# Performance work log

Measured on AMD Instinct MI355X. Metric: run time of the kernel, lower is better.

## Reference

```python
import jax, jax.numpy as jnp
import numpy as np

N = 100000   # nodes
E = 3200000  # edges
C = 256      # in_channels
H = 64       # hidden_channels
G = 512      # graphs in batch
FC = [128, 64, 32, 16]
OUT = 2
EPS = 1e-5


def _linear(key, fan_in, fan_out):
    k1, k2 = jax.random.split(key)
    s = 1.0 / np.sqrt(fan_in)
    W = jax.random.uniform(k1, (fan_in, fan_out), jnp.float32, -s, s)
    b = jax.random.uniform(k2, (fan_out,), jnp.float32, -s, s)
    return W, b


def setup_inputs() -> dict:
    key = jax.random.key(0)
    ks = jax.random.split(key, 12)
    x = jax.random.normal(ks[0], (N, C), jnp.float32)
    edge_index = jax.random.randint(ks[1], (2, E), 0, N, dtype=jnp.int64)
    batch = jnp.sort(jax.random.randint(ks[2], (N,), 0, G, dtype=jnp.int64))
    w1, b1 = _linear(ks[3], C, H)
    w2, b2 = _linear(ks[4], H, H)
    g1 = jnp.ones((H,), jnp.float32); be1 = jnp.zeros((H,), jnp.float32)
    g2 = jnp.ones((H,), jnp.float32); be2 = jnp.zeros((H,), jnp.float32)
    fw1, fb1 = _linear(ks[5], H, FC[0])
    fw2, fb2 = _linear(ks[6], FC[0], FC[1])
    fw3, fb3 = _linear(ks[7], FC[1], FC[2])
    fw4, fb4 = _linear(ks[8], FC[2], FC[3])
    ow, ob = _linear(ks[9], FC[3], OUT)
    return dict(x=x, edge_index=edge_index, batch=batch,
                w1=w1, b1=b1, w2=w2, b2=b2,
                g1=g1, be1=be1, g2=g2, be2=be2,
                fw1=fw1, fb1=fb1, fw2=fw2, fb2=fb2,
                fw3=fw3, fb3=fb3, fw4=fw4, fb4=fb4,
                ow=ow, ob=ob)


def _gcn_layers(x, edge_index, w1, b1, w2, b2, g1, be1, g2, be2):
    # PyG GCNConv: add self loops, symmetric deg^-1/2 normalization, scatter-add at dst
    loops = jnp.arange(N, dtype=edge_index.dtype)
    src = jnp.concatenate([edge_index[0], loops])
    dst = jnp.concatenate([edge_index[1], loops])
    deg = jax.ops.segment_sum(jnp.ones((E + N,), jnp.float32), dst, num_segments=N)
    dis = jnp.where(deg > 0, jax.lax.rsqrt(jnp.maximum(deg, 1.0)), 0.0)
    norm = (dis[src] * dis[dst])[:, None]  # [E+N, 1]

    def conv(h, W, b):
        h = h @ W
        return jax.ops.segment_sum(h[src] * norm, dst, num_segments=N) + b

    def bn(h, g, be):  # BatchNorm1d over node dim (training-mode batch stats)
        m = jnp.mean(h, axis=0)
        v = jnp.var(h, axis=0)
        return (h - m) * jax.lax.rsqrt(v + EPS) * g + be

    h = bn(jax.nn.relu(conv(x, w1, b1)), g1, be1)   # dropout = identity (eval)
    h = bn(jax.nn.relu(conv(h, w2, b2)), g2, be2)
    return h


def reference(x, edge_index, batch, w1, b1, w2, b2, g1, be1, g2, be2,
              fw1, fb1, fw2, fb2, fw3, fb3, fw4, fb4, ow, ob):
    h = _gcn_layers(x, edge_index, w1, b1, w2, b2, g1, be1, g2, be2)
    # global_mean_pool over batch vector
    s = jax.ops.segment_sum(h, batch, num_segments=G)
    cnt = jax.ops.segment_sum(jnp.ones((N,), jnp.float32), batch, num_segments=G)
    p = s / jnp.maximum(cnt, 1.0)[:, None]  # [G, H]
    h = jax.nn.relu(p @ fw1 + fb1)
    h = jax.nn.relu(h @ fw2 + fb2)
    h = jax.nn.relu(h @ fw3 + fb3)
    h = jax.nn.relu(h @ fw4 + fb4)
    return h @ ow + ob  # [G, OUT]
```

## Files before the change

### kernel.cpp

```cpp
#include <hip/hip_runtime.h>
#include <hip/hip_fp16.h>

#define N_NODES 100000
#define E_EDGES 3200000
#define NG      512
#define BN_EPS  1e-5f

#define BSH     7
#define BNODES  128
#define NBUCK   782
#define NCHUNK  1024
#define CHUNK   3125

__global__ __launch_bounds__(256) void k_zero(float* __restrict__ stats1,
                                              float* __restrict__ stats2,
                                              float* __restrict__ sums,
                                              float* __restrict__ cnt) {
  int i = blockIdx.x * 256 + threadIdx.x;
  if (i < 128) { stats1[i] = 0.f; stats2[i] = 0.f; }
  if (i < NG * 64) sums[i] = 0.f;
  if (i < NG) cnt[i] = 0.f;
}

__global__ __launch_bounds__(256) void kb_hist(const int* __restrict__ ei,
                                               int* __restrict__ counts) {
  __shared__ int h[NBUCK];
  const int c = blockIdx.x, tid = threadIdx.x;
  for (int b = tid; b < NBUCK; b += 256) h[b] = 0;
  __syncthreads();
  const int* dst = ei + E_EDGES + c * CHUNK;
  for (int i = tid; i < CHUNK; i += 256) atomicAdd(&h[dst[i] >> BSH], 1);
  __syncthreads();
  for (int b = tid; b < NBUCK; b += 256) counts[b * NCHUNK + c] = h[b];
}

__global__ __launch_bounds__(1024) void kb_scan1(int* __restrict__ counts,
                                                 int* __restrict__ btot) {
  __shared__ int sm[NCHUNK];
  const int b = blockIdx.x, tid = threadIdx.x;
  const int cval = counts[b * NCHUNK + tid];
  int val = cval;
  sm[tid] = val;
  __syncthreads();
  for (int off = 1; off < NCHUNK; off <<= 1) {
    int t = (tid >= off) ? sm[tid - off] : 0;
    __syncthreads();
    val += t;
    sm[tid] = val;
    __syncthreads();
  }
  counts[b * NCHUNK + tid] = val - cval;
  if (tid == NCHUNK - 1) btot[b] = val;
}

__global__ __launch_bounds__(1024) void kb_scan2(const int* __restrict__ btot,
                                                 int* __restrict__ bbase) {
  __shared__ int sm[1024];
  const int tid = threadIdx.x;
  const int cval = (tid < NBUCK) ? btot[tid] : 0;
  int val = cval;
  sm[tid] = val;
  __syncthreads();
  for (int off = 1; off < 1024; off <<= 1) {
    int t = (tid >= off) ? sm[tid - off] : 0;
    __syncthreads();
    val += t;
    sm[tid] = val;
    __syncthreads();
  }
  if (tid < NBUCK) bbase[tid] = val - cval;
  if (tid == NBUCK - 1) bbase[NBUCK] = val;
}

__global__ __launch_bounds__(256) void kb_scatter(const int* __restrict__ ei,
                                                  const int* __restrict__ counts,
                                                  const int* __restrict__ bbase,
                                                  int* __restrict__ binned) {
  __shared__ int cur[NBUCK];
  const int c = blockIdx.x, tid = threadIdx.x;
  for (int b = tid; b < NBUCK; b += 256) cur[b] = bbase[b] + counts[b * NCHUNK + c];
  __syncthreads();
  const int* srcp = ei + c * CHUNK;
  const int* dstp = ei + E_EDGES + c * CHUNK;
  for (int i = tid; i < CHUNK; i += 256) {
    const int s = srcp[i], d = dstp[i];
    const int pos = atomicAdd(&cur[d >> BSH], 1);
    binned[pos] = ((d & (BNODES - 1)) << 17) | s;
  }
}

__global__ __launch_bounds__(256) void kb_degsort(const int* __restrict__ binned,
                                                  const int* __restrict__ bbase,
                                                  int* __restrict__ csr,
                                                  int* __restrict__ row_start,
                                                  float* __restrict__ dis) {
  __shared__ int h[BNODES];
  __shared__ int pre[BNODES];
  const int b = blockIdx.x, tid = threadIdx.x;
  if (tid < BNODES) h[tid] = 0;
  __syncthreads();
  const int e0 = bbase[b], e1 = bbase[b + 1];
  for (int i = e0 + tid; i < e1; i += 256) atomicAdd(&h[binned[i] >> 17], 1);
  __syncthreads();
  if (tid < BNODES) pre[tid] = h[tid];
  __syncthreads();
  for (int off = 1; off < BNODES; off <<= 1) {
    int t = (tid >= off && tid < BNODES) ? pre[tid - off] : 0;
    __syncthreads();
    if (tid < BNODES) pre[tid] += t;
    __syncthreads();
  }
  if (tid < BNODES) {
    const int n = b * BNODES + tid;
    const int ex = e0 + pre[tid] - h[tid];
    if (n < N_NODES) {
      row_start[n] = ex;
      dis[n] = rsqrtf((float)(h[tid] + 1));
    }
    h[tid] = ex;
  }
  if (b == NBUCK - 1 && tid == 0) row_start[N_NODES] = E_EDGES;
  __syncthreads();
  for (int i = e0 + tid; i < e1; i += 256) {
    const int v = binned[i];
    const int pos = atomicAdd(&h[v >> 17], 1);
    csr[pos] = v & 0x1FFFF;
  }
}

template <int K, bool BN>
__global__ __launch_bounds__(256) void k_gemm(const float* __restrict__ in,
                                              const float* __restrict__ W,
                                              const float* __restrict__ dis,
                                              const float* __restrict__ stats,
                                              const float* __restrict__ gam,
                                              const float* __restrict__ bet,
                                              __half* __restrict__ y) {
  __shared__ float xs[64 * 68];
  __shared__ float wsm[64 * 64];
  __shared__ float scv[64], shv[64];
  const int tid = threadIdx.x;
  const int n0 = blockIdx.x * 64;
  const int lane = tid & 63, wv = tid >> 6;
  const int nq = lane & 15;
  const int chb = wv * 16 + (lane >> 4) * 4;
  if (BN) {
    if (tid < 64) {
      const float m = stats[tid] * (1.0f / N_NODES);
      const float v = stats[64 + tid] * (1.0f / N_NODES) - m * m;
      const float sc = rsqrtf(v + BN_EPS) * gam[tid];
      scv[tid] = sc;
      shv[tid] = bet[tid] - m * sc;
    }
  }
  float a[4][4] = {{0,0,0,0},{0,0,0,0},{0,0,0,0},{0,0,0,0}};
  for (int c0 = 0; c0 < K; c0 += 64) {
    __syncthreads();
#pragma unroll
    for (int i = 0; i < 4; ++i) {
      const int idx = tid + i * 256;
      const int n = idx >> 4, c4 = (idx & 15) * 4;
      const int nn = min(n0 + n, N_NODES - 1);
      float4 v = *(const float4*)&in[(size_t)nn * K + c0 + c4];
      if (BN) {
        v.x = v.x * scv[c4] + shv[c4];
        v.y = v.y * scv[c4 + 1] + shv[c4 + 1];
        v.z = v.z * scv[c4 + 2] + shv[c4 + 2];
        v.w = v.w * scv[c4 + 3] + shv[c4 + 3];
      }
      *(float4*)&xs[n * 68 + c4] = v;
    }
#pragma unroll
    for (int i = 0; i < 4; ++i) {
      const int idx = tid + i * 256;
      const int c = idx >> 4, ch4 = (idx & 15) * 4;
      *(float4*)&wsm[c * 64 + ch4] = *(const float4*)&W[(size_t)(c0 + c) * 64 + ch4];
    }
    __syncthreads();
    for (int c = 0; c < 64; c += 4) {
      float wq[4][4];
#pragma unroll
      for (int cc = 0; cc < 4; ++cc) {
        const float4 w4 = *(const float4*)&wsm[(c + cc) * 64 + chb];
        wq[cc][0] = w4.x; wq[cc][1] = w4.y; wq[cc][2] = w4.z; wq[cc][3] = w4.w;
      }
#pragma unroll
      for (int i = 0; i < 4; ++i) {
        const float4 xv = *(const float4*)&xs[(nq + 16 * i) * 68 + c];
#pragma unroll
        for (int j = 0; j < 4; ++j) {
          a[i][j] = fmaf(xv.x, wq[0][j],
                    fmaf(xv.y, wq[1][j],
                    fmaf(xv.z, wq[2][j],
                    fmaf(xv.w, wq[3][j], a[i][j]))));
        }
      }
    }
  }
#pragma unroll
  for (int i = 0; i < 4; ++i) {
    const int n = n0 + nq + 16 * i;
    if (n < N_NODES) {
      const float d = dis[n];
      union { __half h[4]; float2 f; } u;
      u.h[0] = __float2half_rn(d * a[i][0]);
      u.h[1] = __float2half_rn(d * a[i][1]);
      u.h[2] = __float2half_rn(d * a[i][2]);
      u.h[3] = __float2half_rn(d * a[i][3]);
      *(float2*)&y[(size_t)n * 64 + chb] = u.f;
    }
  }
}

template <bool POOL>
__global__ __launch_bounds__(256) void k_gather(const int* __restrict__ csr,
                                                const int* __restrict__ rs,
                                                const __half* __restrict__ y,
                                                const float* __restrict__ dis,
                                                const float* __restrict__ bias,
                                                float* __restrict__ hout,
                                                float* __restrict__ stats,
                                                const int* __restrict__ batch,
                                                float* __restrict__ sums,
                                                float* __restrict__ cnt) {
  const int tid = threadIdx.x;
  const int lane = tid & 63;
  const int p = lane >> 5;
  const int c = lane & 31;
  const int wid = (blockIdx.x * 256 + tid) >> 6;
  const int nw = (gridDim.x * 256) >> 6;
  const int per = (N_NODES + nw - 1) / nw;
  const int n0 = wid * per;
  const int n1 = min(N_NODES, n0 + per);
  const float bx = bias[2 * c], by = bias[2 * c + 1];
  float s1x = 0.f, s1y = 0.f, s2x = 0.f, s2y = 0.f;
  int curg = -1, run = 0;
  float px = 0.f, py = 0.f;
  for (int n = n0; n < n1; ++n) {
    int e = rs[n];
    const int end = rs[n + 1];
    float ax = 0.f, ay = 0.f;
    if (p == 0) {
      const float2 f = __half22float2(*(const __half2*)&y[(size_t)n * 64 + 2 * c]);
      ax = f.x; ay = f.y;
    }
    for (; e + 8 <= end; e += 8) {
      const int i0 = csr[e + p];
      const int i1 = csr[e + 2 + p];
      const int i2 = csr[e + 4 + p];
      const int i3 = csr[e + 6 + p];
      const float2 f0 = __half22float2(*(const __half2*)&y[(size_t)i0 * 64 + 2 * c]);
      const float2 f1 = __half22float2(*(const __half2*)&y[(size_t)i1 * 64 + 2 * c]);
      const float2 f2 = __half22float2(*(const __half2*)&y[(size_t)i2 * 64 + 2 * c]);
      const float2 f3 = __half22float2(*(const __half2*)&y[(size_t)i3 * 64 + 2 * c]);
      ax += (f0.x + f1.x) + (f2.x + f3.x);
      ay += (f0.y + f1.y) + (f2.y + f3.y);
    }
    for (; e + 2 <= end; e += 2) {
      const int i0 = csr[e + p];
      const float2 f = __half22float2(*(const __half2*)&y[(size_t)i0 * 64 + 2 * c]);
      ax += f.x; ay += f.y;
    }
    if (e < end && p == 0) {
      const int i0 = csr[e];
      const float2 f = __half22float2(*(const __half2*)&y[(size_t)i0 * 64 + 2 * c]);
      ax += f.x; ay += f.y;
    }
    ax += __shfl_xor(ax, 32);
    ay += __shfl_xor(ay, 32);
    const float d = dis[n];
    const float vx = fmaxf(d * ax + bx, 0.f);
    const float vy = fmaxf(d * ay + by, 0.f);
    if (lane < 32) {
      if (!POOL) *(float2*)&hout[(size_t)n * 64 + 2 * c] = make_float2(vx, vy);
      s1x += vx; s1y += vy;
      s2x += vx * vx; s2y += vy * vy;
    }
    if (POOL) {
      const int g = batch[n];
      if (g != curg) {
        if (run) {
          if (lane < 32) {
            atomicAdd(&sums[curg * 64 + 2 * c], px);
            atomicAdd(&sums[curg * 64 + 2 * c + 1], py);
          }
          if (lane == 0) atomicAdd(&cnt[curg], (float)run);
        }
        curg = g; run = 0; px = 0.f; py = 0.f;
      }
      if (lane < 32) { px += vx; py += vy; }
      ++run;
    }
  }
  if (POOL && run) {
    if (lane < 32) {
      atomicAdd(&sums[curg * 64 + 2 * c], px);
      atomicAdd(&sums[curg * 64 + 2 * c + 1], py);
    }
    if (lane == 0) atomicAdd(&cnt[curg], (float)run);
  }
  __shared__ float r1[256], r2[256];
  const int wv = tid >> 6;
  if (lane < 32) {
    r1[wv * 64 + 2 * c] = s1x; r1[wv * 64 + 2 * c + 1] = s1y;
    r2[wv * 64 + 2 * c] = s2x; r2[wv * 64 + 2 * c + 1] = s2y;
  }
  __syncthreads();
  if (tid < 64) {
    atomicAdd(&stats[tid], r1[tid] + r1[tid + 64] + r1[tid + 128] + r1[tid + 192]);
  } else if (tid < 128) {
    const int h = tid - 64;
    atomicAdd(&stats[64 + h], r2[h] + r2[h + 64] + r2[h + 128] + r2[h + 192]);
  }
}

__global__ __launch_bounds__(128) void k_mlp(const float* __restrict__ sums,
                                             const float* __restrict__ cnt,
                                             const float* __restrict__ stats,
                                             const float* __restrict__ gam,
                                             const float* __restrict__ bet,
                                             const float* __restrict__ fw1, const float* __restrict__ fb1,
                                             const float* __restrict__ fw2, const float* __restrict__ fb2,
                                             const float* __restrict__ fw3, const float* __restrict__ fb3,
                                             const float* __restrict__ fw4, const float* __restrict__ fb4,
                                             const float* __restrict__ ow, const float* __restrict__ ob,
                                             float* __restrict__ out) {
  __shared__ float u0[128], u1[128];
  const int g = blockIdx.x, t = threadIdx.x;
  if (t < 64) {
    const float m = stats[t] * (1.0f / N_NODES);
    const float v = stats[64 + t] * (1.0f / N_NODES) - m * m;
    const float sc = rsqrtf(v + BN_EPS) * gam[t];
    const float sh = bet[t] - m * sc;
    u0[t] = (sums[g * 64 + t] / fmaxf(cnt[g], 1.0f)) * sc + sh;
  }
  __syncthreads();
  if (t < 128) {
    float a = fb1[t];
    for (int k = 0; k < 64; ++k) a = fmaf(u0[k], fw1[k * 128 + t], a);
    u1[t] = fmaxf(a, 0.f);
  }
  __syncthreads();
  if (t < 64) {
    float a = fb2[t];
    for (int k = 0; k < 128; ++k) a = fmaf(u1[k], fw2[k * 64 + t], a);
    u0[t] = fmaxf(a, 0.f);
  }
  __syncthreads();
  if (t < 32) {
    float a = fb3[t];
    for (int k = 0; k < 64; ++k) a = fmaf(u0[k], fw3[k * 32 + t], a);
    u1[t] = fmaxf(a, 0.f);
  }
  __syncthreads();
  if (t < 16) {
    float a = fb4[t];
    for (int k = 0; k < 32; ++k) a = fmaf(u1[k], fw4[k * 16 + t], a);
    u0[t] = fmaxf(a, 0.f);
  }
  __syncthreads();
  if (t < 2) {
    float a = ob[t];
    for (int k = 0; k < 16; ++k) a = fmaf(u0[k], ow[k * 2 + t], a);
    out[g * 2 + t] = a;
  }
}

extern "C" void kernel_launch(void* const* d_in, const int* in_sizes, int n_in,
                              void* d_out, int out_size, void* d_ws, size_t ws_size,
                              hipStream_t stream) {
  const float* x    = (const float*)d_in[0];
  const int*   ei   = (const int*)d_in[1];
  const int*   batch= (const int*)d_in[2];
  const float* w1   = (const float*)d_in[3];
  const float* b1   = (const float*)d_in[4];
  const float* w2   = (const float*)d_in[5];
  const float* b2   = (const float*)d_in[6];
  const float* g1   = (const float*)d_in[7];
  const float* be1  = (const float*)d_in[8];
  const float* g2   = (const float*)d_in[9];
  const float* be2  = (const float*)d_in[10];
  const float* fw1  = (const float*)d_in[11]; const float* fb1 = (const float*)d_in[12];
  const float* fw2  = (const float*)d_in[13]; const float* fb2 = (const float*)d_in[14];
  const float* fw3  = (const float*)d_in[15]; const float* fb3 = (const float*)d_in[16];
  const float* fw4  = (const float*)d_in[17]; const float* fb4 = (const float*)d_in[18];
  const float* ow   = (const float*)d_in[19]; const float* ob  = (const float*)d_in[20];
  float* out = (float*)d_out;

  char* ws = (char*)d_ws;
  auto alloc = [&](size_t bytes) {
    void* p = ws;
    ws += (bytes + 255) & ~(size_t)255;
    return p;
  };
  float*  dis      = (float*)alloc((size_t)N_NODES * 4);
  int*    counts   = (int*)  alloc((size_t)NBUCK * NCHUNK * 4);
  int*    btot     = (int*)  alloc((size_t)NBUCK * 4);
  int*    bbase    = (int*)  alloc((size_t)(NBUCK + 1) * 4);
  int*    binned   = (int*)  alloc((size_t)E_EDGES * 4);
  int*    csr      = (int*)  alloc((size_t)E_EDGES * 4);
  int*    row_start= (int*)  alloc((size_t)(N_NODES + 1) * 4);
  __half* yH       = (__half*)alloc((size_t)N_NODES * 64 * 2);
  float*  hB       = (float*)alloc((size_t)N_NODES * 64 * 4);
  float*  stats1   = (float*)alloc(512);
  float*  stats2   = (float*)alloc(512);
  float*  sums     = (float*)alloc((size_t)NG * 64 * 4);
  float*  cnt      = (float*)alloc((size_t)NG * 4);

  const int nblkG = (N_NODES + 63) / 64;

  k_zero    <<<128, 256, 0, stream>>>(stats1, stats2, sums, cnt);
  kb_hist   <<<NCHUNK, 256, 0, stream>>>(ei, counts);
  kb_scan1  <<<NBUCK, NCHUNK, 0, stream>>>(counts, btot);
  kb_scan2  <<<1, 1024, 0, stream>>>(btot, bbase);
  kb_scatter<<<NCHUNK, 256, 0, stream>>>(ei, counts, bbase, binned);
  kb_degsort<<<NBUCK, 256, 0, stream>>>(binned, bbase, csr, row_start, dis);

  k_gemm<256, false><<<nblkG, 256, 0, stream>>>(x, w1, dis, nullptr, nullptr, nullptr, yH);
  k_gather<false><<<2048, 256, 0, stream>>>(csr, row_start, yH, dis, b1, hB, stats1,
                                            nullptr, nullptr, nullptr);

  k_gemm<64, true><<<nblkG, 256, 0, stream>>>(hB, w2, dis, stats1, g1, be1, yH);
  k_gather<true><<<2048, 256, 0, stream>>>(csr, row_start, yH, dis, b2, nullptr, stats2,
                                           batch, sums, cnt);

  k_mlp<<<NG, 128, 0, stream>>>(sums, cnt, stats2, g2, be2,
                                fw1, fb1, fw2, fb2, fw3, fb3, fw4, fb4, ow, ob, out);
}
```

Measured before the change: 600.6 us.

## Gather fp16 rows with 16-byte loads over 8 edges per wave

Changes the per-node gather so each lane loads 8 half-precision channels with one 16-byte load, and a wave covers 8 edges in parallel instead of 2 with 4-byte loads. Partial sums across the 8 edge groups are combined with a three-step butterfly shuffle that ends with each lane owning one channel, so all 64 lanes write outputs and stats. This cuts the number of load instructions per gathered row and raises memory-level parallelism on the random neighbour reads. In exchange it adds shuffle and select work per node and wastes lanes on nodes with few neighbours.

```diff
diff --git a/kernel.cpp b/kernel.cpp
--- a/kernel.cpp
+++ b/kernel.cpp
@@ -225,86 +225,114 @@
                                                 float* __restrict__ cnt) {
   const int tid = threadIdx.x;
   const int lane = tid & 63;
-  const int p = lane >> 5;
-  const int c = lane & 31;
+  const int p = lane >> 3;
+  const int c8 = lane & 7;
+  const int ch = c8 * 8 + ((p & 1) << 2) + (p & 2) + ((p >> 2) & 1);
   const int wid = (blockIdx.x * 256 + tid) >> 6;
   const int nw = (gridDim.x * 256) >> 6;
   const int per = (N_NODES + nw - 1) / nw;
   const int n0 = wid * per;
   const int n1 = min(N_NODES, n0 + per);
-  const float bx = bias[2 * c], by = bias[2 * c + 1];
-  float s1x = 0.f, s1y = 0.f, s2x = 0.f, s2y = 0.f;
+  const float bch = bias[ch];
+  float s1 = 0.f, s2 = 0.f;
   int curg = -1, run = 0;
-  float px = 0.f, py = 0.f;
+  float px = 0.f;
+  union U8 { float4 f4; __half2 h2[4]; };
   for (int n = n0; n < n1; ++n) {
     int e = rs[n];
     const int end = rs[n + 1];
-    float ax = 0.f, ay = 0.f;
+    float acc[8] = {0.f, 0.f, 0.f, 0.f, 0.f, 0.f, 0.f, 0.f};
     if (p == 0) {
-      const float2 f = __half22float2(*(const __half2*)&y[(size_t)n * 64 + 2 * c]);
-      ax = f.x; ay = f.y;
+      U8 u;
+      u.f4 = *(const float4*)&y[(size_t)n * 64 + c8 * 8];
+#pragma unroll
+      for (int q = 0; q < 4; ++q) {
+        const float2 f = __half22float2(u.h2[q]);
+        acc[2 * q] += f.x;
+        acc[2 * q + 1] += f.y;
+      }
+    }
+    for (; e + 16 <= end; e += 16) {
+      const int ia = csr[e + p];
+      const int ib = csr[e + 8 + p];
+      U8 ua, ub;
+      ua.f4 = *(const float4*)&y[(size_t)ia * 64 + c8 * 8];
+      ub.f4 = *(const float4*)&y[(size_t)ib * 64 + c8 * 8];
+#pragma unroll
+      for (int q = 0; q < 4; ++q) {
+        const float2 fa = __half22float2(ua.h2[q]);
+        const float2 fb = __half22float2(ub.h2[q]);
+        acc[2 * q] += fa.x + fb.x;
+        acc[2 * q + 1] += fa.y + fb.y;
+      }
     }
     for (; e + 8 <= end; e += 8) {
-      const int i0 = csr[e + p];
-      const int i1 = csr[e + 2 + p];
-      const int i2 = csr[e + 4 + p];
-      const int i3 = csr[e + 6 + p];
-      const float2 f0 = __half22float2(*(const __half2*)&y[(size_t)i0 * 64 + 2 * c]);
-      const float2 f1 = __half22float2(*(const __half2*)&y[(size_t)i1 * 64 + 2 * c]);
-      const float2 f2 = __half22float2(*(const __half2*)&y[(size_t)i2 * 64 + 2 * c]);
-      const float2 f3 = __half22float2(*(const __half2*)&y[(size_t)i3 * 64 + 2 * c]);
-      ax += (f0.x + f1.x) + (f2.x + f3.x);
-      ay += (f0.y + f1.y) + (f2.y + f3.y);
-    }
-    for (; e + 2 <= end; e += 2) {
-      const int i0 = csr[e + p];
-      const float2 f = __half22float2(*(const __half2*)&y[(size_t)i0 * 64 + 2 * c]);
-      ax += f.x; ay += f.y;
-    }
-    if (e < end && p == 0) {
-      const int i0 = csr[e];
-      const float2 f = __half22float2(*(const __half2*)&y[(size_t)i0 * 64 + 2 * c]);
-      ax += f.x; ay += f.y;
-    }
-    ax += __shfl_xor(ax, 32);
-    ay += __shfl_xor(ay, 32);
-    const float d = dis[n];
-    const float vx = fmaxf(d * ax + bx, 0.f);
-    const float vy = fmaxf(d * ay + by, 0.f);
-    if (lane < 32) {
-      if (!POOL) *(float2*)&hout[(size_t)n * 64 + 2 * c] = make_float2(vx, vy);
-      s1x += vx; s1y += vy;
-      s2x += vx * vx; s2y += vy * vy;
-    }
+      const int ia = csr[e + p];
+      U8 ua;
+      ua.f4 = *(const float4*)&y[(size_t)ia * 64 + c8 * 8];
+#pragma unroll
+      for (int q = 0; q < 4; ++q) {
+        const float2 fa = __half22float2(ua.h2[q]);
+        acc[2 * q] += fa.x;
+        acc[2 * q + 1] += fa.y;
+      }
+    }
+    if (e < end) {
+      const int rem = end - e;
+      const int i0 = csr[(p < rem) ? e + p : e];
+      U8 u;
+      u.f4 = *(const float4*)&y[(size_t)i0 * 64 + c8 * 8];
+      if (p < rem) {
+#pragma unroll
+        for (int q = 0; q < 4; ++q) {
+          const float2 f = __half22float2(u.h2[q]);
+          acc[2 * q] += f.x;
+          acc[2 * q + 1] += f.y;
+        }
+      }
+    }
+    float t[4];
+#pragma unroll
+    for (int j = 0; j < 4; ++j) {
+      const float send = (p & 1) ? acc[j] : acc[4 + j];
+      const float keep = (p & 1) ? acc[4 + j] : acc[j];
+      t[j] = keep + __shfl_xor(send, 8);
+    }
+    float u2[2];
+#pragma unroll
+    for (int j = 0; j < 2; ++j) {
+      const float send = (p & 2) ? t[j] : t[2 + j];
+      const float keep = (p & 2) ? t[2 + j] : t[j];
+      u2[j] = keep + __shfl_xor(send, 16);
+    }
+    const float send3 = (p & 4) ? u2[0] : u2[1];
+    const float keep3 = (p & 4) ? u2[1] : u2[0];
+    const float s = keep3 + __shfl_xor(send3, 32);
+    const float v = fmaxf(dis[n] * s + bch, 0.f);
+    if (!POOL) hout[(size_t)n * 64 + ch] = v;
+    s1 += v;
+    s2 += v * v;
     if (POOL) {
       const int g = batch[n];
       if (g != curg) {
         if (run) {
-          if (lane < 32) {
-            atomicAdd(&sums[curg * 64 + 2 * c], px);
-            atomicAdd(&sums[curg * 64 + 2 * c + 1], py);
-          }
+          atomicAdd(&sums[curg * 64 + ch], px);
           if (lane == 0) atomicAdd(&cnt[curg], (float)run);
         }
-        curg = g; run = 0; px = 0.f; py = 0.f;
-      }
-      if (lane < 32) { px += vx; py += vy; }
+        curg = g; run = 0; px = 0.f;
+      }
+      px += v;
       ++run;
     }
   }
   if (POOL && run) {
-    if (lane < 32) {
-      atomicAdd(&sums[curg * 64 + 2 * c], px);
-      atomicAdd(&sums[curg * 64 + 2 * c + 1], py);
-    }
+    atomicAdd(&sums[curg * 64 + ch], px);
     if (lane == 0) atomicAdd(&cnt[curg], (float)run);
   }
   __shared__ float r1[256], r2[256];
   const int wv = tid >> 6;
-  if (lane < 32) {
-    r1[wv * 64 + 2 * c] = s1x; r1[wv * 64 + 2 * c + 1] = s1y;
-    r2[wv * 64 + 2 * c] = s2x; r2[wv * 64 + 2 * c + 1] = s2y;
-  }
+  r1[wv * 64 + ch] = s1;
+  r2[wv * 64 + ch] = s2;
   __syncthreads();
   if (tid < 64) {
     atomicAdd(&stats[tid], r1[tid] + r1[tid + 64] + r1[tid + 128] + r1[tid + 192]);
```

After: 568.8 us. -5.3%, faster.

## Split gather into channel slices with 16 edges per wave iteration

Applied to the files above, without the earlier changes.

Rewrites the neighbour-aggregation kernel so each block works on one of four 16-channel slices. Each lane loads 8 bytes (four halves) for one of 16 edges at a time, instead of two lanes per edge covering all 64 channels. The aim is to keep more independent neighbour loads in flight and shrink each block's per-row working set of the feature table. The cost is that CSR indices and the per-node loop run four times, once per slice. The block-to-slice and node-range mapping is hardcoded for a fixed grid size, so it depends on the launch matching it.

```diff
diff --git a/kernel.cpp b/kernel.cpp
--- a/kernel.cpp
+++ b/kernel.cpp
@@ -223,94 +223,124 @@
                                                 const int* __restrict__ batch,
                                                 float* __restrict__ sums,
                                                 float* __restrict__ cnt) {
-  const int tid = threadIdx.x;
+  const int tid  = threadIdx.x;
   const int lane = tid & 63;
-  const int p = lane >> 5;
-  const int c = lane & 31;
-  const int wid = (blockIdx.x * 256 + tid) >> 6;
-  const int nw = (gridDim.x * 256) >> 6;
-  const int per = (N_NODES + nw - 1) / nw;
-  const int n0 = wid * per;
-  const int n1 = min(N_NODES, n0 + per);
-  const float bx = bias[2 * c], by = bias[2 * c + 1];
-  float s1x = 0.f, s1y = 0.f, s2x = 0.f, s2y = 0.f;
+  const int slot = lane >> 2;
+  const int cq   = lane & 3;
+  const int slice = (blockIdx.x & 7) >> 1;
+  const int sbase = slice * 16;
+  const int chl  = cq * 4 + (slot & 3);
+  const int ch   = sbase + chl;
+  const int j    = ((blockIdx.x >> 3) << 1) | (blockIdx.x & 1);
+  const int wid  = j * 4 + (tid >> 6);
+  const int per  = (N_NODES + 2047) / 2048;
+  const int n0   = wid * per;
+  const int n1   = min(N_NODES, n0 + per);
+  const float bch = bias[ch];
+  const __half* yb = y + sbase + cq * 4;
+  float s1 = 0.f, s2 = 0.f;
   int curg = -1, run = 0;
-  float px = 0.f, py = 0.f;
+  float px = 0.f;
+  union U4 { float2 f2; __half2 h2[2]; };
   for (int n = n0; n < n1; ++n) {
     int e = rs[n];
     const int end = rs[n + 1];
-    float ax = 0.f, ay = 0.f;
-    if (p == 0) {
-      const float2 f = __half22float2(*(const __half2*)&y[(size_t)n * 64 + 2 * c]);
-      ax = f.x; ay = f.y;
-    }
-    for (; e + 8 <= end; e += 8) {
-      const int i0 = csr[e + p];
-      const int i1 = csr[e + 2 + p];
-      const int i2 = csr[e + 4 + p];
-      const int i3 = csr[e + 6 + p];
-      const float2 f0 = __half22float2(*(const __half2*)&y[(size_t)i0 * 64 + 2 * c]);
-      const float2 f1 = __half22float2(*(const __half2*)&y[(size_t)i1 * 64 + 2 * c]);
-      const float2 f2 = __half22float2(*(const __half2*)&y[(size_t)i2 * 64 + 2 * c]);
-      const float2 f3 = __half22float2(*(const __half2*)&y[(size_t)i3 * 64 + 2 * c]);
-      ax += (f0.x + f1.x) + (f2.x + f3.x);
-      ay += (f0.y + f1.y) + (f2.y + f3.y);
-    }
-    for (; e + 2 <= end; e += 2) {
-      const int i0 = csr[e + p];
-      const float2 f = __half22float2(*(const __half2*)&y[(size_t)i0 * 64 + 2 * c]);
-      ax += f.x; ay += f.y;
-    }
-    if (e < end && p == 0) {
-      const int i0 = csr[e];
-      const float2 f = __half22float2(*(const __half2*)&y[(size_t)i0 * 64 + 2 * c]);
-      ax += f.x; ay += f.y;
-    }
-    ax += __shfl_xor(ax, 32);
-    ay += __shfl_xor(ay, 32);
-    const float d = dis[n];
-    const float vx = fmaxf(d * ax + bx, 0.f);
-    const float vy = fmaxf(d * ay + by, 0.f);
-    if (lane < 32) {
-      if (!POOL) *(float2*)&hout[(size_t)n * 64 + 2 * c] = make_float2(vx, vy);
-      s1x += vx; s1y += vy;
-      s2x += vx * vx; s2y += vy * vy;
+    float a0 = 0.f, a1 = 0.f, a2 = 0.f, a3 = 0.f;
+    if (slot == 0) {
+      U4 u;
+      u.f2 = *(const float2*)&yb[(size_t)n * 64];
+      const float2 f0 = __half22float2(u.h2[0]);
+      const float2 f1 = __half22float2(u.h2[1]);
+      a0 += f0.x; a1 += f0.y; a2 += f1.x; a3 += f1.y;
+    }
+    for (; e + 32 <= end; e += 32) {
+      const int ia = __builtin_nontemporal_load(&csr[e + slot]);
+      const int ib = __builtin_nontemporal_load(&csr[e + 16 + slot]);
+      U4 ua, ub;
+      ua.f2 = *(const float2*)&yb[(size_t)ia * 64];
+      ub.f2 = *(const float2*)&yb[(size_t)ib * 64];
+      const float2 fa0 = __half22float2(ua.h2[0]);
+      const float2 fa1 = __half22float2(ua.h2[1]);
+      const float2 fb0 = __half22float2(ub.h2[0]);
+      const float2 fb1 = __half22float2(ub.h2[1]);
+      a0 += fa0.x + fb0.x; a1 += fa0.y + fb0.y;
+      a2 += fa1.x + fb1.x; a3 += fa1.y + fb1.y;
+    }
+    for (; e + 16 <= end; e += 16) {
+      const int ia = __builtin_nontemporal_load(&csr[e + slot]);
+      U4 ua;
+      ua.f2 = *(const float2*)&yb[(size_t)ia * 64];
+      const float2 fa0 = __half22float2(ua.h2[0]);
+      const float2 fa1 = __half22float2(ua.h2[1]);
+      a0 += fa0.x; a1 += fa0.y; a2 += fa1.x; a3 += fa1.y;
+    }
+    if (e < end) {
+      const int rem = end - e;
+      const int ia = __builtin_nontemporal_load(&csr[slot < rem ? e + slot : e]);
+      U4 u;
+      u.f2 = *(const float2*)&yb[(size_t)ia * 64];
+      if (slot < rem) {
+        const float2 f0 = __half22float2(u.h2[0]);
+        const float2 f1 = __half22float2(u.h2[1]);
+        a0 += f0.x; a1 += f0.y; a2 += f1.x; a3 += f1.y;
+      }
+    }
+    a0 += __shfl_xor(a0, 32); a1 += __shfl_xor(a1, 32);
+    a2 += __shfl_xor(a2, 32); a3 += __shfl_xor(a3, 32);
+    a0 += __shfl_xor(a0, 16); a1 += __shfl_xor(a1, 16);
+    a2 += __shfl_xor(a2, 16); a3 += __shfl_xor(a3, 16);
+    float t0, t1;
+    {
+      const bool hi = (slot & 2) != 0;
+      const float sd0 = hi ? a0 : a2;
+      const float sd1 = hi ? a1 : a3;
+      const float kp0 = hi ? a2 : a0;
+      const float kp1 = hi ? a3 : a1;
+      t0 = kp0 + __shfl_xor(sd0, 8);
+      t1 = kp1 + __shfl_xor(sd1, 8);
+    }
+    float s;
+    {
+      const bool hi = (slot & 1) != 0;
+      const float sd = hi ? t0 : t1;
+      const float kp = hi ? t1 : t0;
+      s = kp + __shfl_xor(sd, 4);
+    }
+    const float v = fmaxf(dis[n] * s + bch, 0.f);
+    if (lane < 16) {
+      if (!POOL) __builtin_nontemporal_store(v, &hout[(size_t)n * 64 + ch]);
+      s1 += v;
+      s2 += v * v;
     }
     if (POOL) {
       const int g = batch[n];
       if (g != curg) {
         if (run) {
-          if (lane < 32) {
-            atomicAdd(&sums[curg * 64 + 2 * c], px);
-            atomicAdd(&sums[curg * 64 + 2 * c + 1], py);
-          }
-          if (lane == 0) atomicAdd(&cnt[curg], (float)run);
+          if (lane < 16) atomicAdd(&sums[curg * 64 + ch], px);
+          if (lane == 0 && slice == 0) atomicAdd(&cnt[curg], (float)run);
         }
-        curg = g; run = 0; px = 0.f; py = 0.f;
+        curg = g; run = 0; px = 0.f;
       }
-      if (lane < 32) { px += vx; py += vy; }
+      if (lane < 16) px += v;
       ++run;
     }
   }
   if (POOL && run) {
-    if (lane < 32) {
-      atomicAdd(&sums[curg * 64 + 2 * c], px);
-      atomicAdd(&sums[curg * 64 + 2 * c + 1], py);
-    }
-    if (lane == 0) atomicAdd(&cnt[curg], (float)run);
-  }
-  __shared__ float r1[256], r2[256];
+    if (lane < 16) atomicAdd(&sums[curg * 64 + ch], px);
+    if (lane == 0 && slice == 0) atomicAdd(&cnt[curg], (float)run);
+  }
+  __shared__ float r1[64], r2[64];
   const int wv = tid >> 6;
-  if (lane < 32) {
-    r1[wv * 64 + 2 * c] = s1x; r1[wv * 64 + 2 * c + 1] = s1y;
-    r2[wv * 64 + 2 * c] = s2x; r2[wv * 64 + 2 * c + 1] = s2y;
-  }
-  __syncthreads();
-  if (tid < 64) {
-    atomicAdd(&stats[tid], r1[tid] + r1[tid + 64] + r1[tid + 128] + r1[tid + 192]);
-  } else if (tid < 128) {
-    const int h = tid - 64;
-    atomicAdd(&stats[64 + h], r2[h] + r2[h + 64] + r2[h + 128] + r2[h + 192]);
+  if (lane < 16) {
+    r1[wv * 16 + chl] = s1;
+    r2[wv * 16 + chl] = s2;
+  }
+  __syncthreads();
+  if (tid < 16) {
+    atomicAdd(&stats[sbase + tid], r1[tid] + r1[tid + 16] + r1[tid + 32] + r1[tid + 48]);
+  } else if (tid < 32) {
+    const int h = tid - 16;
+    atomicAdd(&stats[64 + sbase + h], r2[h] + r2[h + 16] + r2[h + 32] + r2[h + 48]);
   }
 }
 
```

Result: slower. 777.7 us (+29.5%).
